# Kernel tuning notes

Hardware: AMD Instinct MI355X
Metric: run time of the kernel (lower is better)

## Reference

```python
import jax, jax.numpy as jnp
import numpy as np

M, B, D_IN, D_HID, D_OUT = 8, 4096, 1024, 4096, 1024

def setup_inputs() -> dict:
    key = jax.random.key(0)
    ks = jax.random.split(key, 4)
    x = jax.random.normal(ks[0], (B, D_IN), dtype=jnp.float32)
    route = jax.random.randint(ks[1], (B,), 0, M, dtype=jnp.int64)
    # branch params (scaled like standard inits)
    W1 = jax.random.normal(ks[2], (M, D_IN, D_HID), dtype=jnp.float32) / np.sqrt(D_IN)
    b1 = jnp.zeros((M, D_HID), dtype=jnp.float32)
    W2 = jax.random.normal(ks[3], (M, D_HID, D_OUT), dtype=jnp.float32) / np.sqrt(D_HID)
    b2 = jnp.zeros((M, D_OUT), dtype=jnp.float32)
    return {"x": x, "route": route, "W1": W1, "b1": b1, "W2": W2, "b2": b2}

def reference(x, route, W1, b1, W2, b2):
    # Faithful to the dense compute-all-branches-then-one-hot-select pattern.
    # h: [M, B, D_HID] — every branch computed for every sample
    h = jax.nn.gelu(jnp.einsum('bd,mdh->mbh', x, W1) + b1[:, None, :])
    stacked = jnp.einsum('mbh,mho->mbo', h, W2) + b2[:, None, :]  # [M, B, D_OUT]
    one_hot = jax.nn.one_hot(route, M, dtype=stacked.dtype)       # [B, M]
    selected = jnp.einsum('mbd,bm->bd', stacked, one_hot)         # [B, D_OUT]
    return selected
```

## Files before the change

### kernel.cpp

```cpp
#include <hip/hip_runtime.h>
#include <math.h>

#define MEXP 8
#define BTOK 4096
#define DIN  1024
#define DHID 4096
#define DOUT 1024
#define BK   32

typedef __bf16 bf16x4 __attribute__((ext_vector_type(4)));
typedef __bf16 bf16x8 __attribute__((ext_vector_type(8)));
typedef float  f32x4  __attribute__((ext_vector_type(4)));

__device__ __forceinline__ void gld16(const void* g, void* l) {
    __builtin_amdgcn_global_load_lds(
        (const __attribute__((address_space(1))) unsigned int*)g,
        (__attribute__((address_space(3))) unsigned int*)l, 16, 0, 0);
}

__device__ __forceinline__ float gelu_tanh(float v) {
    float t = 1.5957691216057308f * v * (1.0f + 0.044715f * v * v);
    return v / (1.0f + __expf(-t));
}

__global__ void route_kernel(const int* __restrict__ route, int* __restrict__ perm,
                             int* __restrict__ offsets) {
    __shared__ int cnt[MEXP];
    __shared__ int off[MEXP + 1];
    int t = threadIdx.x;
    if (t < MEXP) cnt[t] = 0;
    __syncthreads();
    for (int i = t; i < BTOK; i += blockDim.x) atomicAdd(&cnt[route[i]], 1);
    __syncthreads();
    if (t == 0) {
        int s = 0;
        for (int m = 0; m < MEXP; m++) { off[m] = s; s += cnt[m]; }
        off[MEXP] = s;
    }
    __syncthreads();
    if (t < MEXP + 1) offsets[t] = off[t];
    if (t < MEXP) cnt[t] = off[t];
    __syncthreads();
    for (int i = t; i < BTOK; i += blockDim.x) {
        int p = atomicAdd(&cnt[route[i]], 1);
        perm[p] = i;
    }
}

__global__ __launch_bounds__(256) void convert_x_kernel(const float* __restrict__ x,
                                                        __bf16* __restrict__ xb) {
    int i = blockIdx.x * 256 + threadIdx.x;
    float4 v = *(const float4*)(x + (size_t)i * 4);
    bf16x4 p;
    p[0] = (__bf16)v.x; p[1] = (__bf16)v.y; p[2] = (__bf16)v.z; p[3] = (__bf16)v.w;
    *(bf16x4*)(xb + (size_t)i * 4) = p;
}

template <int K, int N>
__global__ __launch_bounds__(256) void transpose_kernel(const float* __restrict__ W,
                                                        __bf16* __restrict__ Wt) {
    __shared__ float T[64][132];
    int m = blockIdx.z;
    int k0 = blockIdx.y * 64;
    int n0 = blockIdx.x * 128;
    const float* Wm = W + (size_t)m * K * N;
    __bf16* Wtm = Wt + (size_t)m * N * K;
    int t = threadIdx.x;
    int nc4 = (t & 31) * 4;
    int kr0 = t >> 5;
#pragma unroll
    for (int it = 0; it < 8; it++) {
        int kr = it * 8 + kr0;
        float4 v = *(const float4*)(Wm + (size_t)(k0 + kr) * N + n0 + nc4);
        *(float4*)&T[kr][nc4] = v;
    }
    __syncthreads();
#pragma unroll
    for (int it = 0; it < 4; it++) {
        int task = it * 256 + t;
        int nr = task >> 3;
        int gr = task & 7;
        bf16x8 v;
#pragma unroll
        for (int j = 0; j < 8; j++) {
            int j2 = (j + gr) & 7;
            v[j2] = (__bf16)T[gr * 8 + j2][nr];
        }
        *(bf16x8*)(Wtm + (size_t)(n0 + nr) * K + k0 + gr * 8) = v;
    }
}

#define GEMM_STAGE(ABUF, BBUF)                                                          \
    do {                                                                                \
        bf16x8 af[4], bfr[4];                                                           \
        _Pragma("unroll") for (int i = 0; i < 4; i++)                                   \
            af[i] = *(bf16x8*)&(ABUF)[(wr + i * 16 + lm) * BK + quad * 8];              \
        _Pragma("unroll") for (int j = 0; j < 4; j++)                                   \
            bfr[j] = *(bf16x8*)&(BBUF)[(wc + j * 16 + lm) * BK + quad * 8];             \
        _Pragma("unroll") for (int i = 0; i < 4; i++)                                   \
            _Pragma("unroll") for (int j = 0; j < 4; j++)                               \
                acc[i][j] = __builtin_amdgcn_mfma_f32_16x16x32_bf16(af[i], bfr[j],      \
                                                                   acc[i][j], 0, 0, 0);\
    } while (0)

#define PREFETCH(buf, kk)                                                               \
    do {                                                                                \
        gld16(gA[0] + (kk), lA[0] + (buf) * 8192);                                      \
        gld16(gA[1] + (kk), lA[1] + (buf) * 8192);                                      \
        gld16(gB[0] + (kk), lB[0] + (buf) * 8192);                                      \
        gld16(gB[1] + (kk), lB[1] + (buf) * 8192);                                      \
    } while (0)

__global__ __launch_bounds__(256)
void gemm1_kernel(const __bf16* __restrict__ xb, const __bf16* __restrict__ W1t,
                  const float* __restrict__ b1, const int* __restrict__ perm,
                  const int* __restrict__ offsets, __bf16* __restrict__ H) {
    int m = blockIdx.z;
    int seg_start = offsets[m];
    int cnt = offsets[m + 1] - seg_start;
    int row0 = blockIdx.y * 128;
    if (row0 >= cnt) return;
    int col0 = blockIdx.x * 128;

    __shared__ __bf16 As[2][128 * BK];
    __shared__ __bf16 Bs[2][128 * BK];

    int tid = threadIdx.x;
    int wave = tid >> 6, lane = tid & 63;
    int wr = (wave >> 1) * 64, wc = (wave & 1) * 64;
    int lm = lane & 15, quad = lane >> 4;

    const __bf16* gA[2];
    char* lA[2];
    const __bf16* gB[2];
    char* lB[2];
    const __bf16* Wm = W1t + (size_t)m * DHID * DIN;
#pragma unroll
    for (int c = 0; c < 2; c++) {
        int rA = row0 + wave * 32 + c * 16 + (lane >> 2);
        int tok = perm[seg_start + (rA < cnt ? rA : cnt - 1)];
        gA[c] = xb + (size_t)tok * DIN + (lane & 3) * 8;
        lA[c] = (char*)&As[0][0] + (wave * 32 + c * 16) * 64 + lane * 16;
        int nB = col0 + wave * 32 + c * 16 + (lane >> 2);
        gB[c] = Wm + (size_t)nB * DIN + (lane & 3) * 8;
        lB[c] = (char*)&Bs[0][0] + (wave * 32 + c * 16) * 64 + lane * 16;
    }

    f32x4 acc[4][4];
#pragma unroll
    for (int i = 0; i < 4; i++)
#pragma unroll
        for (int j = 0; j < 4; j++)
#pragma unroll
            for (int r = 0; r < 4; r++) acc[i][j][r] = 0.0f;

    const int NIT = DIN / BK;
    PREFETCH(0, 0);
    for (int it = 0; it < NIT; it += 2) {
        __syncthreads();
        if (it + 1 < NIT) PREFETCH(1, (it + 1) * BK);
        GEMM_STAGE(As[0], Bs[0]);
        __syncthreads();
        if (it + 2 < NIT) PREFETCH(0, (it + 2) * BK);
        GEMM_STAGE(As[1], Bs[1]);
    }

#pragma unroll
    for (int j = 0; j < 4; j++) {
        int col = col0 + wc + j * 16 + lm;
        float bias = b1[m * DHID + col];
#pragma unroll
        for (int i = 0; i < 4; i++) {
#pragma unroll
            for (int r = 0; r < 4; r++) {
                int row = row0 + wr + i * 16 + quad * 4 + r;
                if (row < cnt) {
                    float v = acc[i][j][r] + bias;
                    H[(size_t)(seg_start + row) * DHID + col] = (__bf16)gelu_tanh(v);
                }
            }
        }
    }
}

__global__ __launch_bounds__(256)
void gemm2p_kernel(const __bf16* __restrict__ H, const __bf16* __restrict__ W2t,
                   const int* __restrict__ offsets, float* __restrict__ partial) {
    int m = blockIdx.z >> 2;
    int s = blockIdx.z & 3;
    int seg_start = offsets[m];
    int cnt = offsets[m + 1] - seg_start;
    int row0 = blockIdx.y * 128;
    if (row0 >= cnt) return;
    int col0 = blockIdx.x * 128;
    int kbase = s * (DHID / 4);

    __shared__ __bf16 As[2][128 * BK];
    __shared__ __bf16 Bs[2][128 * BK];

    int tid = threadIdx.x;
    int wave = tid >> 6, lane = tid & 63;
    int wr = (wave >> 1) * 64, wc = (wave & 1) * 64;
    int lm = lane & 15, quad = lane >> 4;

    const __bf16* gA[2];
    char* lA[2];
    const __bf16* gB[2];
    char* lB[2];
    const __bf16* Wm = W2t + (size_t)m * DOUT * DHID;
#pragma unroll
    for (int c = 0; c < 2; c++) {
        int rA = row0 + wave * 32 + c * 16 + (lane >> 2);
        int hr = seg_start + (rA < cnt ? rA : cnt - 1);
        gA[c] = H + (size_t)hr * DHID + kbase + (lane & 3) * 8;
        lA[c] = (char*)&As[0][0] + (wave * 32 + c * 16) * 64 + lane * 16;
        int nB = col0 + wave * 32 + c * 16 + (lane >> 2);
        gB[c] = Wm + (size_t)nB * DHID + kbase + (lane & 3) * 8;
        lB[c] = (char*)&Bs[0][0] + (wave * 32 + c * 16) * 64 + lane * 16;
    }

    f32x4 acc[4][4];
#pragma unroll
    for (int i = 0; i < 4; i++)
#pragma unroll
        for (int j = 0; j < 4; j++)
#pragma unroll
            for (int r = 0; r < 4; r++) acc[i][j][r] = 0.0f;

    const int NIT = (DHID / 4) / BK;
    PREFETCH(0, 0);
    for (int it = 0; it < NIT; it += 2) {
        __syncthreads();
        if (it + 1 < NIT) PREFETCH(1, (it + 1) * BK);
        GEMM_STAGE(As[0], Bs[0]);
        __syncthreads();
        if (it + 2 < NIT) PREFETCH(0, (it + 2) * BK);
        GEMM_STAGE(As[1], Bs[1]);
    }

    float* pdst = partial + (size_t)s * BTOK * DOUT;
#pragma unroll
    for (int j = 0; j < 4; j++) {
        int col = col0 + wc + j * 16 + lm;
#pragma unroll
        for (int i = 0; i < 4; i++) {
#pragma unroll
            for (int r = 0; r < 4; r++) {
                int row = row0 + wr + i * 16 + quad * 4 + r;
                if (row < cnt)
                    pdst[(size_t)(seg_start + row) * DOUT + col] = acc[i][j][r];
            }
        }
    }
}

__global__ __launch_bounds__(256)
void reduce_kernel(const float* __restrict__ partial, const int* __restrict__ perm,
                   const int* __restrict__ offsets, const float* __restrict__ b2,
                   float* __restrict__ out) {
    int r = blockIdx.x;
    int c4 = threadIdx.x * 4;
    int e = 0;
#pragma unroll
    for (int q = 0; q < MEXP - 1; q++)
        if (r >= offsets[q + 1]) e = q + 1;
    int tok = perm[r];
    float4 o = *(const float4*)(b2 + e * DOUT + c4);
#pragma unroll
    for (int s = 0; s < 4; s++) {
        float4 a = *(const float4*)(partial + (size_t)(s * BTOK + r) * DOUT + c4);
        o.x += a.x; o.y += a.y; o.z += a.z; o.w += a.w;
    }
    *(float4*)(out + (size_t)tok * DOUT + c4) = o;
}

extern "C" void kernel_launch(void* const* d_in, const int* in_sizes, int n_in,
                              void* d_out, int out_size, void* d_ws, size_t ws_size,
                              hipStream_t stream) {
    const float* x     = (const float*)d_in[0];
    const int*   route = (const int*)d_in[1];
    const float* W1    = (const float*)d_in[2];
    const float* b1    = (const float*)d_in[3];
    const float* W2    = (const float*)d_in[4];
    const float* b2    = (const float*)d_in[5];
    float* out = (float*)d_out;

    char* ws = (char*)d_ws;
    int*    perm    = (int*)ws;
    int*    offsets = (int*)(ws + 16384);
    __bf16* xb      = (__bf16*)(ws + 32768);
    __bf16* H       = (__bf16*)(ws + 32768 + (8ull << 20));
    __bf16* Wt1     = (__bf16*)(ws + 32768 + (40ull << 20));
    __bf16* Wt2     = (__bf16*)(ws + 32768 + (104ull << 20));
    float*  partial = (float*)(ws + 32768 + (40ull << 20));

    route_kernel<<<1, 256, 0, stream>>>(route, perm, offsets);
    convert_x_kernel<<<(BTOK * DIN / 4) / 256, 256, 0, stream>>>(x, xb);
    transpose_kernel<DIN, DHID><<<dim3(DHID / 128, DIN / 64, MEXP), 256, 0, stream>>>(W1, Wt1);
    transpose_kernel<DHID, DOUT><<<dim3(DOUT / 128, DHID / 64, MEXP), 256, 0, stream>>>(W2, Wt2);
    gemm1_kernel<<<dim3(DHID / 128, 8, MEXP), 256, 0, stream>>>(xb, Wt1, b1, perm, offsets, H);
    gemm2p_kernel<<<dim3(DOUT / 128, 8, MEXP * 4), 256, 0, stream>>>(H, Wt2, offsets, partial);
    reduce_kernel<<<BTOK, 256, 0, stream>>>(partial, perm, offsets, b2, out);
}
```

Measured before the change: 507.4 us.

## Swizzle block order for XCD locality and stage GEMM1 epilogue through LDS

Both GEMM kernels remap the flat block index so that consecutive logical tiles of one expert land on the same XCD, which is meant to improve L2 reuse of expert weights across the chiplets. The GEMM1 epilogue now writes GELU outputs into a swizzled LDS tile and then does coalesced 16-byte stores to H, replacing scattered 2-byte global stores. The W2 transpose launch is also moved after GEMM1. This costs extra shared-memory traffic and two more barriers.

```diff
diff --git a/kernel.cpp b/kernel.cpp
--- a/kernel.cpp
+++ b/kernel.cpp
@@ -90,13 +90,13 @@
     }
 }
 
-#define GEMM_STAGE(ABUF, BBUF)                                                          \
+#define GEMM_STAGE(Ap, Bp)                                                              \
     do {                                                                                \
         bf16x8 af[4], bfr[4];                                                           \
         _Pragma("unroll") for (int i = 0; i < 4; i++)                                   \
-            af[i] = *(bf16x8*)&(ABUF)[(wr + i * 16 + lm) * BK + quad * 8];              \
+            af[i] = *(bf16x8*)&(Ap)[(wr + i * 16 + lm) * BK + quad * 8];                \
         _Pragma("unroll") for (int j = 0; j < 4; j++)                                   \
-            bfr[j] = *(bf16x8*)&(BBUF)[(wc + j * 16 + lm) * BK + quad * 8];             \
+            bfr[j] = *(bf16x8*)&(Bp)[(wc + j * 16 + lm) * BK + quad * 8];               \
         _Pragma("unroll") for (int i = 0; i < 4; i++)                                   \
             _Pragma("unroll") for (int j = 0; j < 4; j++)                               \
                 acc[i][j] = __builtin_amdgcn_mfma_f32_16x16x32_bf16(af[i], bfr[j],      \
@@ -115,15 +115,21 @@
 void gemm1_kernel(const __bf16* __restrict__ xb, const __bf16* __restrict__ W1t,
                   const float* __restrict__ b1, const int* __restrict__ perm,
                   const int* __restrict__ offsets, __bf16* __restrict__ H) {
-    int m = blockIdx.z;
+    int flat = blockIdx.x + 32 * (blockIdx.y + 8 * blockIdx.z);
+    int logical = (flat & 7) * 256 + (flat >> 3);
+    int m  = logical >> 8;
+    int bx = (logical >> 3) & 31;
+    int by = logical & 7;
+
     int seg_start = offsets[m];
     int cnt = offsets[m + 1] - seg_start;
-    int row0 = blockIdx.y * 128;
+    int row0 = by * 128;
     if (row0 >= cnt) return;
-    int col0 = blockIdx.x * 128;
-
-    __shared__ __bf16 As[2][128 * BK];
-    __shared__ __bf16 Bs[2][128 * BK];
+    int col0 = bx * 128;
+
+    __shared__ char smem[32768];
+    __bf16* As = (__bf16*)smem;
+    __bf16* Bs = (__bf16*)(smem + 16384);
 
     int tid = threadIdx.x;
     int wave = tid >> 6, lane = tid & 63;
@@ -140,10 +146,10 @@
         int rA = row0 + wave * 32 + c * 16 + (lane >> 2);
         int tok = perm[seg_start + (rA < cnt ? rA : cnt - 1)];
         gA[c] = xb + (size_t)tok * DIN + (lane & 3) * 8;
-        lA[c] = (char*)&As[0][0] + (wave * 32 + c * 16) * 64 + lane * 16;
+        lA[c] = smem + (wave * 32 + c * 16) * 64 + lane * 16;
         int nB = col0 + wave * 32 + c * 16 + (lane >> 2);
         gB[c] = Wm + (size_t)nB * DIN + (lane & 3) * 8;
-        lB[c] = (char*)&Bs[0][0] + (wave * 32 + c * 16) * 64 + lane * 16;
+        lB[c] = smem + 16384 + (wave * 32 + c * 16) * 64 + lane * 16;
     }
 
     f32x4 acc[4][4];
@@ -159,26 +165,38 @@
     for (int it = 0; it < NIT; it += 2) {
         __syncthreads();
         if (it + 1 < NIT) PREFETCH(1, (it + 1) * BK);
-        GEMM_STAGE(As[0], Bs[0]);
+        GEMM_STAGE(As, Bs);
         __syncthreads();
         if (it + 2 < NIT) PREFETCH(0, (it + 2) * BK);
-        GEMM_STAGE(As[1], Bs[1]);
-    }
-
+        GEMM_STAGE(As + 4096, Bs + 4096);
+    }
+
+    __syncthreads();
+    __bf16* Ct = (__bf16*)smem;
 #pragma unroll
     for (int j = 0; j < 4; j++) {
-        int col = col0 + wc + j * 16 + lm;
-        float bias = b1[m * DHID + col];
+        int col = wc + j * 16 + lm;
+        float bias = b1[m * DHID + col0 + col];
 #pragma unroll
         for (int i = 0; i < 4; i++) {
 #pragma unroll
             for (int r = 0; r < 4; r++) {
-                int row = row0 + wr + i * 16 + quad * 4 + r;
-                if (row < cnt) {
-                    float v = acc[i][j][r] + bias;
-                    H[(size_t)(seg_start + row) * DHID + col] = (__bf16)gelu_tanh(v);
-                }
+                int row = wr + i * 16 + quad * 4 + r;
+                float v = acc[i][j][r] + bias;
+                Ct[row * 128 + (col ^ ((row & 7) << 3))] = (__bf16)gelu_tanh(v);
             }
+        }
+    }
+    __syncthreads();
+#pragma unroll
+    for (int it = 0; it < 8; it++) {
+        int idx = it * 256 + tid;
+        int row = idx >> 4;
+        int c = idx & 15;
+        int grow = row0 + row;
+        if (grow < cnt) {
+            bf16x8 v = *(bf16x8*)&Ct[row * 128 + ((c * 8) ^ ((row & 7) << 3))];
+            *(bf16x8*)(H + (size_t)(seg_start + grow) * DHID + col0 + c * 8) = v;
         }
     }
 }
@@ -186,13 +204,18 @@
 __global__ __launch_bounds__(256)
 void gemm2p_kernel(const __bf16* __restrict__ H, const __bf16* __restrict__ W2t,
                    const int* __restrict__ offsets, float* __restrict__ partial) {
-    int m = blockIdx.z >> 2;
-    int s = blockIdx.z & 3;
+    int flat = blockIdx.x + 8 * (blockIdx.y + 8 * blockIdx.z);
+    int logical = (flat & 7) * 256 + (flat >> 3);
+    int m  = logical >> 8;
+    int s  = (logical >> 6) & 3;
+    int bx = (logical >> 3) & 7;
+    int by = logical & 7;
+
     int seg_start = offsets[m];
     int cnt = offsets[m + 1] - seg_start;
-    int row0 = blockIdx.y * 128;
+    int row0 = by * 128;
     if (row0 >= cnt) return;
-    int col0 = blockIdx.x * 128;
+    int col0 = bx * 128;
     int kbase = s * (DHID / 4);
 
     __shared__ __bf16 As[2][128 * BK];
@@ -297,8 +320,8 @@
     route_kernel<<<1, 256, 0, stream>>>(route, perm, offsets);
     convert_x_kernel<<<(BTOK * DIN / 4) / 256, 256, 0, stream>>>(x, xb);
     transpose_kernel<DIN, DHID><<<dim3(DHID / 128, DIN / 64, MEXP), 256, 0, stream>>>(W1, Wt1);
+    gemm1_kernel<<<dim3(DHID / 128, 8, MEXP), 256, 0, stream>>>(xb, Wt1, b1, perm, offsets, H);
     transpose_kernel<DHID, DOUT><<<dim3(DOUT / 128, DHID / 64, MEXP), 256, 0, stream>>>(W2, Wt2);
-    gemm1_kernel<<<dim3(DHID / 128, 8, MEXP), 256, 0, stream>>>(xb, Wt1, b1, perm, offsets, H);
     gemm2p_kernel<<<dim3(DOUT / 128, 8, MEXP * 4), 256, 0, stream>>>(H, Wt2, offsets, partial);
     reduce_kernel<<<BTOK, 256, 0, stream>>>(partial, perm, offsets, b2, out);
 }
```

Result: no change. 512.6 us (+1.0%).
